# Performance work log

Hardware: AMD Instinct MI355X
Metric: run time of the kernel (lower is better)

The kernel has to match this reference:

```python
import jax, jax.numpy as jnp
import numpy as np
from jax import lax

B, T, D_IN = 512, 128, 512
HID, C = 256, 96
MAX_LEN = 25  # num_steps = MAX_LEN + 1


def setup_inputs() -> dict:
    key = jax.random.key(0)
    ks = jax.random.split(key, 12)
    num_steps = MAX_LEN + 1
    gru_in = D_IN + C
    inp = {
        "batch_H": jax.random.normal(ks[0], (B, T, D_IN), dtype=jnp.float32),
        "text": jax.random.randint(ks[1], (B, num_steps), 0, C, dtype=jnp.int64),
        "batch_max_length": MAX_LEN,
        # attention params
        "W_i2h": jax.random.normal(ks[2], (HID, D_IN), dtype=jnp.float32) * 0.04,
        "W_h2h": jax.random.normal(ks[3], (HID, HID), dtype=jnp.float32) * 0.06,
        "b_h2h": jnp.zeros((HID,), dtype=jnp.float32),
        "W_score": jax.random.normal(ks[4], (1, HID), dtype=jnp.float32) * 0.08,
        # GRUCell params (torch layout: [3H, in], gate order r, z, n)
        "W_ih": jax.random.normal(ks[5], (3 * HID, gru_in), dtype=jnp.float32) * 0.04,
        "W_hh": jax.random.normal(ks[6], (3 * HID, HID), dtype=jnp.float32) * 0.06,
        "b_ih": jnp.zeros((3 * HID,), dtype=jnp.float32),
        "b_hh": jnp.zeros((3 * HID,), dtype=jnp.float32),
        # generator
        "W_gen": jax.random.normal(ks[7], (C, HID), dtype=jnp.float32) * 0.07,
        "b_gen": jnp.zeros((C,), dtype=jnp.float32),
    }
    return inp


def reference(batch_H, text, batch_max_length, W_i2h, W_h2h, b_h2h, W_score,
              W_ih, W_hh, b_ih, b_hh, W_gen, b_gen):
    num_steps = batch_max_length + 1
    hid = W_h2h.shape[0]
    n_cls = W_gen.shape[0]
    dtype = batch_H.dtype
    bsz = batch_H.shape[0]

    # i2h(batch_H) is loop-invariant: [B, T, H]
    H_proj = jnp.einsum("btd,hd->bth", batch_H, W_i2h)

    def step(hidden, char_ids):
        # additive attention
        h_proj = hidden @ W_h2h.T + b_h2h                      # [B, H]
        e = jnp.tanh(H_proj + h_proj[:, None, :]) @ W_score[0]  # [B, T]
        alpha = jax.nn.softmax(e, axis=1)                       # [B, T]
        context = jnp.einsum("bt,btd->bd", alpha, batch_H)      # [B, D]
        onehot = jax.nn.one_hot(char_ids, n_cls, dtype=dtype)
        x = jnp.concatenate([context, onehot], axis=1)
        # GRUCell (torch semantics)
        gi = x @ W_ih.T + b_ih
        gh = hidden @ W_hh.T + b_hh
        i_r, i_z, i_n = jnp.split(gi, 3, axis=1)
        h_r, h_z, h_n = jnp.split(gh, 3, axis=1)
        r = jax.nn.sigmoid(i_r + h_r)
        z = jax.nn.sigmoid(i_z + h_z)
        n = jnp.tanh(i_n + r * h_n)
        new_h = (1.0 - z) * n + z * hidden
        return new_h, new_h

    h0 = jnp.zeros((bsz, hid), dtype=dtype)
    chars = jnp.swapaxes(text[:, :num_steps], 0, 1)  # [num_steps, B]
    _, hiddens = lax.scan(step, h0, chars)           # [num_steps, B, H]
    hiddens = jnp.swapaxes(hiddens, 0, 1)            # [B, num_steps, H]
    probs = hiddens @ W_gen.T + b_gen                # [B, num_steps, C]
    return probs
```

## Files before the change

kernel.cpp:

```cpp
#include <hip/hip_runtime.h>

#define BATCH 512
#define TLEN 128
#define DIN 512
#define HID 256
#define NCLS 96
#define STEPS 26
#define GRUIN 608
#define G3 768

#define BM 64
#define BN 64
#define BK 16
#define LDS_STRIDE 68

typedef unsigned short ushort_t;
typedef __attribute__((ext_vector_type(8))) short short8v;
typedef __attribute__((ext_vector_type(4))) float f32x4;
typedef __attribute__((ext_vector_type(8))) unsigned short ushort8v;

__device__ __forceinline__ float fast_tanh(float x) {
    return 1.f - 2.f / (__expf(2.f * x) + 1.f);
}
__device__ __forceinline__ float fast_sigmoid(float x) {
    return 1.f / (1.f + __expf(-x));
}
__device__ __forceinline__ ushort_t f2bf_rne(float f) {
    unsigned int u = __float_as_uint(f);
    unsigned int r = (u + 0x7FFFu + ((u >> 16) & 1u)) >> 16;
    return (ushort_t)r;
}
__device__ __forceinline__ float bf2f(ushort_t h) {
    return __uint_as_float(((unsigned int)h) << 16);
}

__global__ __launch_bounds__(256)
void prep_all(const float* __restrict__ W_h2h, const float* __restrict__ W_hh,
              const float* __restrict__ W_ih, const float* __restrict__ W_i2h,
              const float* __restrict__ b_ih, const float* __restrict__ b_h2h,
              const float* __restrict__ b_hh, const float* __restrict__ W_gen,
              ushort_t* __restrict__ Wcat16, ushort_t* __restrict__ B16cat,
              float* __restrict__ WembT, ushort_t* __restrict__ Wgen16,
              float* __restrict__ bcat, float* __restrict__ hidden,
              float* __restrict__ hg) {
    int idx = blockIdx.x * 256 + threadIdx.x;
    if (idx < 262144) {
        int n = idx >> 8, k = idx & 255;
        float v = (n < 256) ? W_h2h[n * 256 + k] : W_hh[(size_t)(n - 256) * 256 + k];
        Wcat16[idx] = f2bf_rne(v);
    } else if (idx < 262144 + 524288) {
        int j = idx - 262144;
        int r = j >> 9, c = j & 511;
        float v = (r < 768) ? W_ih[(size_t)r * GRUIN + c] : W_i2h[(size_t)(r - 768) * 512 + c];
        B16cat[j] = f2bf_rne(v);
    } else if (idx < 262144 + 524288 + 73728) {
        int j = idx - (262144 + 524288);
        int ch = j / 768, jj = j - ch * 768;
        WembT[j] = W_ih[(size_t)jj * GRUIN + 512 + ch] + b_ih[jj];
    } else if (idx < 262144 + 524288 + 73728 + 24576) {
        int j = idx - (262144 + 524288 + 73728);
        Wgen16[j] = f2bf_rne(W_gen[j]);
    } else if (idx < 262144 + 524288 + 73728 + 24576 + 1024) {
        int j = idx - (262144 + 524288 + 73728 + 24576);
        bcat[j] = (j < 256) ? b_h2h[j] : b_hh[j - 256];
    } else if (idx < 262144 + 524288 + 73728 + 24576 + 1024 + 131072) {
        int j = idx - (262144 + 524288 + 73728 + 24576 + 1024);
        hidden[j] = 0.f;
    } else if (idx < 262144 + 524288 + 73728 + 24576 + 1024 + 131072 + 524288) {
        int j = idx - (262144 + 524288 + 73728 + 24576 + 1024 + 131072);
        int c = j & 1023;
        hg[j] = (c < 256) ? b_h2h[c] : b_hh[c - 256];
    }
}

__global__ __launch_bounds__(256)
void conv_a16(const float* __restrict__ src, ushort_t* __restrict__ dst, int n8) {
    int i = blockIdx.x * 256 + threadIdx.x;
    const int stride = gridDim.x * 256;
    for (; i < n8; i += stride) {
        float4 v0 = ((const float4*)src)[2 * i];
        float4 v1 = ((const float4*)src)[2 * i + 1];
        ushort8v o;
        o[0] = f2bf_rne(v0.x); o[1] = f2bf_rne(v0.y);
        o[2] = f2bf_rne(v0.z); o[3] = f2bf_rne(v0.w);
        o[4] = f2bf_rne(v1.x); o[5] = f2bf_rne(v1.y);
        o[6] = f2bf_rne(v1.z); o[7] = f2bf_rne(v1.w);
        ((ushort8v*)dst)[i] = o;
    }
}

__device__ __forceinline__ int swz(int row, int col8) {
    return (row * 32 + col8 * 8) ^ ((row & 7) << 3);
}

__global__ __launch_bounds__(256)
void hwhp_mfma(const ushort_t* __restrict__ A16,
               const ushort_t* __restrict__ B16,
               ushort_t* __restrict__ HW16,
               ushort_t* __restrict__ Hp16) {
    __shared__ ushort_t As[128 * 32];
    __shared__ ushort_t Bs[128 * 32];
    const int wgid = blockIdx.x;
    const int mt = (wgid & 7) + ((wgid >> 6) << 3);
    const int nt = (wgid >> 3) & 7;
    const int bm = mt * 128, bn = nt * 128;
    const int tid = threadIdx.x;
    const int wid = tid >> 6, lane = tid & 63;
    const int wr = wid >> 1, wc = wid & 1;
    f32x4 acc[4][4] = {};
    const int l15 = lane & 15, lhi = lane >> 4;
    const int rin = (lane >> 2) ^ ((lane >> 4) & 1);
    const int qsrc = (lane & 3) ^ (rin & 3);
    for (int k0 = 0; k0 < 512; k0 += 32) {
        __syncthreads();
#pragma unroll
        for (int c = 0; c < 2; ++c) {
            const int chunk = wid + 4 * c;
            const int row = chunk * 16 + rin;
            __builtin_amdgcn_global_load_lds(
                (const __attribute__((address_space(1))) void*)(A16 + (size_t)(bm + row) * 512 + k0 + qsrc * 8),
                (__attribute__((address_space(3))) void*)(As + chunk * 512),
                16, 0, 0);
            __builtin_amdgcn_global_load_lds(
                (const __attribute__((address_space(1))) void*)(B16 + (size_t)(bn + row) * 512 + k0 + qsrc * 8),
                (__attribute__((address_space(3))) void*)(Bs + chunk * 512),
                16, 0, 0);
        }
        __syncthreads();
        short8v af[4], bfr[4];
#pragma unroll
        for (int i = 0; i < 4; ++i) {
            int arow = wr * 64 + i * 16 + l15;
            af[i] = *(const short8v*)(&As[swz(arow, lhi)]);
            int brow = wc * 64 + i * 16 + l15;
            bfr[i] = *(const short8v*)(&Bs[swz(brow, lhi)]);
        }
#pragma unroll
        for (int i = 0; i < 4; ++i)
#pragma unroll
            for (int j = 0; j < 4; ++j)
                acc[i][j] = __builtin_amdgcn_mfma_f32_16x16x32_bf16(af[i], bfr[j], acc[i][j], 0, 0, 0);
    }
    const int cr0 = bm + wr * 64 + lhi * 4;
    const int cc0 = bn + wc * 64 + l15;
    const bool isHW = (bn < 768);
    ushort_t* outp = isHW ? HW16 : Hp16;
    const int ld = isHW ? 768 : 256;
    const int coff = isHW ? 0 : 768;
#pragma unroll
    for (int i = 0; i < 4; ++i)
#pragma unroll
        for (int j = 0; j < 4; ++j)
#pragma unroll
            for (int p = 0; p < 4; ++p)
                outp[(size_t)(cr0 + i * 16 + p) * ld + (cc0 + j * 16 - coff)] = f2bf_rne(acc[i][j][p]);
}

__global__ __launch_bounds__(256)
void hg_mfma(const ushort_t* __restrict__ H16,
             const ushort_t* __restrict__ W16,
             const float* __restrict__ bcat,
             float* __restrict__ hg) {
    __shared__ ushort_t As[64 * 32];
    __shared__ ushort_t Bs[128 * 32];
    const int wgid = blockIdx.x;
    const int mt = wgid >> 3;
    const int nt = wgid & 7;
    const int bm = mt * 64, bn = nt * 128;
    const int tid = threadIdx.x;
    const int wid = tid >> 6, lane = tid & 63;
    const int wr = wid >> 1, wc = wid & 1;
    const int sr = tid >> 2, sq = tid & 3;
    f32x4 acc[2][4] = {};
    const int l15 = lane & 15, lhi = lane >> 4;
    for (int k0 = 0; k0 < 256; k0 += 32) {
        ushort8v a0 = *(const ushort8v*)(H16 + (size_t)(bm + (sr & 63)) * 256 + k0 + sq * 8);
        ushort8v b0 = *(const ushort8v*)(W16 + (size_t)(bn + sr) * 256 + k0 + sq * 8);
        ushort8v b1 = *(const ushort8v*)(W16 + (size_t)(bn + sr + 64) * 256 + k0 + sq * 8);
        __syncthreads();
        if (sr < 64) *(ushort8v*)(&As[swz(sr, sq)]) = a0;
        *(ushort8v*)(&Bs[swz(sr, sq)]) = b0;
        *(ushort8v*)(&Bs[swz(sr + 64, sq)]) = b1;
        __syncthreads();
        short8v af[2], bfr[4];
#pragma unroll
        for (int i = 0; i < 2; ++i) {
            int arow = wr * 32 + i * 16 + l15;
            af[i] = *(const short8v*)(&As[swz(arow, lhi)]);
        }
#pragma unroll
        for (int j = 0; j < 4; ++j) {
            int brow = wc * 64 + j * 16 + l15;
            bfr[j] = *(const short8v*)(&Bs[swz(brow, lhi)]);
        }
#pragma unroll
        for (int i = 0; i < 2; ++i)
#pragma unroll
            for (int j = 0; j < 4; ++j)
                acc[i][j] = __builtin_amdgcn_mfma_f32_16x16x32_bf16(af[i], bfr[j], acc[i][j], 0, 0, 0);
    }
    const int cr0 = bm + wr * 32 + lhi * 4;
    const int cc0 = bn + wc * 64 + l15;
#pragma unroll
    for (int j = 0; j < 4; ++j) {
        const int c = cc0 + j * 16;
        const float bj = bcat[c];
#pragma unroll
        for (int i = 0; i < 2; ++i)
#pragma unroll
            for (int p = 0; p < 4; ++p)
                hg[(size_t)(cr0 + i * 16 + p) * 1024 + c] = acc[i][j][p] + bj;
    }
}

__global__ __launch_bounds__(1024, 8)
void step_fused(const ushort_t* __restrict__ HW16,
                const ushort_t* __restrict__ Hp16,
                const float* __restrict__ hg,
                const float* __restrict__ WembT,
                const ushort_t* __restrict__ Wgen16,
                const float* __restrict__ Wscore,
                const float* __restrict__ b_gen,
                const int* __restrict__ text,
                int s,
                float* __restrict__ hidden,
                ushort_t* __restrict__ hidden16,
                float* __restrict__ out) {
    const int b = blockIdx.x;
    const int tid = threadIdx.x;
    const int wave = tid >> 6, lane = tid & 63;

    __shared__ __align__(16) float hp[HID];
    __shared__ __align__(16) float wsc[HID];
    __shared__ __align__(16) float parts[6144];
    __shared__ __align__(16) float gi_l[G3];
    __shared__ __align__(16) float sh[HID];
    __shared__ float es[TLEN];
    __shared__ float al[TLEN];
    __shared__ float red[16];

    const size_t rowbase = (size_t)b * TLEN;
    if (tid < 256) {
        hp[tid] = hg[(size_t)b * 1024 + tid];
        wsc[tid] = Wscore[tid];
    }
    __syncthreads();

#pragma unroll
    for (int i = 0; i < 8; ++i) {
        int t = i * 16 + wave;
        ushort4 hv = *(const ushort4*)(Hp16 + (rowbase + t) * 256 + lane * 4);
        float4 hpv = *(const float4*)(&hp[lane * 4]);
        float4 wv = *(const float4*)(&wsc[lane * 4]);
        float sc = fast_tanh(bf2f(hv.x) + hpv.x) * wv.x
                 + fast_tanh(bf2f(hv.y) + hpv.y) * wv.y
                 + fast_tanh(bf2f(hv.z) + hpv.z) * wv.z
                 + fast_tanh(bf2f(hv.w) + hpv.w) * wv.w;
#pragma unroll
        for (int off = 32; off >= 1; off >>= 1) sc += __shfl_xor(sc, off);
        if (lane == 0) es[t] = sc;
    }
    __syncthreads();
    float ev = 0.f, p = 0.f;
    if (tid < TLEN) {
        ev = es[tid];
        float mx = ev;
#pragma unroll
        for (int off = 32; off >= 1; off >>= 1) mx = fmaxf(mx, __shfl_xor(mx, off));
        if (lane == 0) red[wave] = mx;
    }
    __syncthreads();
    if (tid < TLEN) {
        float m = fmaxf(red[0], red[1]);
        p = __expf(ev - m);
        float sm = p;
#pragma unroll
        for (int off = 32; off >= 1; off >>= 1) sm += __shfl_xor(sm, off);
        if (lane == 0) red[8 + wave] = sm;
    }
    __syncthreads();
    if (tid < TLEN) al[tid] = p / (red[8] + red[9]);
    __syncthreads();
    {
        const int tg = tid >> 7;
        const int cq = tid & 127;
        if (cq < 96) {
            float a0 = 0.f, a1 = 0.f, a2 = 0.f, a3 = 0.f;
            float a4 = 0.f, a5 = 0.f, a6 = 0.f, a7 = 0.f;
            const ushort_t* base = HW16 + (rowbase + tg * 16) * 768 + cq * 8;
            const float* alh = &al[tg * 16];
#pragma unroll 4
            for (int i = 0; i < 16; ++i) {
                ushort8v v = *(const ushort8v*)(base + (size_t)i * 768);
                float a = alh[i];
                a0 = fmaf(a, bf2f(v[0]), a0);
                a1 = fmaf(a, bf2f(v[1]), a1);
                a2 = fmaf(a, bf2f(v[2]), a2);
                a3 = fmaf(a, bf2f(v[3]), a3);
                a4 = fmaf(a, bf2f(v[4]), a4);
                a5 = fmaf(a, bf2f(v[5]), a5);
                a6 = fmaf(a, bf2f(v[6]), a6);
                a7 = fmaf(a, bf2f(v[7]), a7);
            }
            float* pr = &parts[tg * 768 + cq * 8];
            pr[0] = a0; pr[1] = a1; pr[2] = a2; pr[3] = a3;
            pr[4] = a4; pr[5] = a5; pr[6] = a6; pr[7] = a7;
        }
    }
    __syncthreads();
    if (tid < G3) {
        float g = parts[tid] + parts[768 + tid] + parts[1536 + tid] + parts[2304 + tid]
                + parts[3072 + tid] + parts[3840 + tid] + parts[4608 + tid] + parts[5376 + tid];
        gi_l[tid] = g;
    }
    __syncthreads();
    if (tid < 256) {
        const int ch = text[b * STEPS + s];
        const float* em = WembT + (size_t)ch * G3;
        const float* ghb = hg + (size_t)b * 1024 + 256;
        float ir = gi_l[tid]       + em[tid]       + ghb[tid];
        float iz = gi_l[256 + tid] + em[256 + tid] + ghb[256 + tid];
        float in_ = gi_l[512 + tid] + em[512 + tid];
        float hn = ghb[512 + tid];
        float rr = fast_sigmoid(ir);
        float zz = fast_sigmoid(iz);
        float nn = fast_tanh(in_ + rr * hn);
        float nh = (1.f - zz) * nn + zz * hidden[(size_t)b * HID + tid];
        hidden[(size_t)b * HID + tid] = nh;
        hidden16[(size_t)b * HID + tid] = f2bf_rne(nh);
        sh[tid] = nh;
    }
    __syncthreads();
    if (tid < NCLS) {
        const ushort_t* wrow = Wgen16 + (size_t)tid * HID;
        float acc = b_gen[tid];
#pragma unroll 4
        for (int k = 0; k < HID; k += 8) {
            ushort8v w8 = *(const ushort8v*)(wrow + k);
            acc = fmaf(sh[k],     bf2f(w8[0]), acc);
            acc = fmaf(sh[k + 1], bf2f(w8[1]), acc);
            acc = fmaf(sh[k + 2], bf2f(w8[2]), acc);
            acc = fmaf(sh[k + 3], bf2f(w8[3]), acc);
            acc = fmaf(sh[k + 4], bf2f(w8[4]), acc);
            acc = fmaf(sh[k + 5], bf2f(w8[5]), acc);
            acc = fmaf(sh[k + 6], bf2f(w8[6]), acc);
            acc = fmaf(sh[k + 7], bf2f(w8[7]), acc);
        }
        out[((size_t)b * STEPS + s) * NCLS + tid] = acc;
    }
}

template <typename OutT>
__device__ __forceinline__ void store_c(OutT* p, float v);
template <> __device__ __forceinline__ void store_c<float>(float* p, float v) { *p = v; }
template <> __device__ __forceinline__ void store_c<ushort_t>(ushort_t* p, float v) { *p = f2bf_rne(v); }

template <typename OutT>
__global__ __launch_bounds__(256)
void gemm_nt(const float* __restrict__ A, int lda,
             const float* __restrict__ Bw, int ldb,
             OutT* __restrict__ Cc, int ldc,
             const float* __restrict__ bias,
             int M, int N, int K) {
    __shared__ float As[BK][LDS_STRIDE];
    __shared__ float Bs[BK][LDS_STRIDE];
    const int tid = threadIdx.x;
    const int bm = blockIdx.x * BM;
    const int bn = blockIdx.y * BN;
    const int tx = tid & 15, ty = tid >> 4;
    const int lr = tid >> 2;
    const int lc = (tid & 3) << 2;
    float acc[4][4] = {};
    const int gr = bm + lr;
    const int gn = bn + lr;
    const float* Arow = A + (size_t)gr * lda;
    const float* Brow = Bw + (size_t)gn * ldb;
    for (int k0 = 0; k0 < K; k0 += BK) {
        float4 va = make_float4(0.f, 0.f, 0.f, 0.f);
        float4 vb = make_float4(0.f, 0.f, 0.f, 0.f);
        if (gr < M) va = *(const float4*)(Arow + k0 + lc);
        if (gn < N) vb = *(const float4*)(Brow + k0 + lc);
        As[lc + 0][lr] = va.x; As[lc + 1][lr] = va.y;
        As[lc + 2][lr] = va.z; As[lc + 3][lr] = va.w;
        Bs[lc + 0][lr] = vb.x; Bs[lc + 1][lr] = vb.y;
        Bs[lc + 2][lr] = vb.z; Bs[lc + 3][lr] = vb.w;
        __syncthreads();
#pragma unroll
        for (int k = 0; k < BK; ++k) {
            float4 a4 = *(const float4*)(&As[k][ty << 2]);
            float4 b4 = *(const float4*)(&Bs[k][tx << 2]);
            float a[4] = {a4.x, a4.y, a4.z, a4.w};
            float b[4] = {b4.x, b4.y, b4.z, b4.w};
#pragma unroll
            for (int i = 0; i < 4; ++i)
#pragma unroll
                for (int j = 0; j < 4; ++j)
                    acc[i][j] = fmaf(a[i], b[j], acc[i][j]);
        }
        __syncthreads();
    }
#pragma unroll
    for (int i = 0; i < 4; ++i) {
        int m = bm + (ty << 2) + i;
        if (m >= M) continue;
#pragma unroll
        for (int j = 0; j < 4; ++j) {
            int n = bn + (tx << 2) + j;
            if (n < N) store_c(&Cc[(size_t)m * ldc + n], acc[i][j] + (bias ? bias[n] : 0.f));
        }
    }
}

__global__ __launch_bounds__(256)
void prep_wcat(const float* __restrict__ W_h2h, const float* __restrict__ W_hh,
               const float* __restrict__ b_h2h, const float* __restrict__ b_hh,
               float* __restrict__ Wcat, float* __restrict__ bcat,
               float* __restrict__ hidden) {
    int idx = blockIdx.x * 256 + threadIdx.x;
    int r = idx >> 8, c = idx & 255;
    Wcat[idx] = (r < 256) ? W_h2h[r * 256 + c] : W_hh[(r - 256) * 256 + c];
    if (idx < 1024) bcat[idx] = (idx < 256) ? b_h2h[idx] : b_hh[idx - 256];
    if (idx < BATCH * HID) hidden[idx] = 0.f;
}

template <typename HT>
__global__ __launch_bounds__(256)
void attn_step(const HT* __restrict__ Hproj,
               const float* __restrict__ batchH,
               const float* __restrict__ hg,
               const float* __restrict__ Wscore,
               float* __restrict__ context) {
    const int b = blockIdx.x;
    const int tid = threadIdx.x;
    __shared__ float hp[HID];
    __shared__ float wsc[HID];
    __shared__ float es[TLEN];
    __shared__ float red[16];
    hp[tid] = hg[b * 1024 + tid];
    wsc[tid] = Wscore[tid];
    __syncthreads();
    const int wave = tid >> 6;
    const int lane = tid & 63;
    const HT* Hp = Hproj + (size_t)b * TLEN * HID;
    for (int t = wave; t < TLEN; t += 4) {
        float x0, x1, x2, x3;
        if constexpr (sizeof(HT) == 4) {
            float4 hv = *(const float4*)((const float*)Hp + (size_t)t * HID + (lane << 2));
            x0 = hv.x; x1 = hv.y; x2 = hv.z; x3 = hv.w;
        } else {
            ushort4 hv = *(const ushort4*)((const ushort_t*)Hp + (size_t)t * HID + (lane << 2));
            x0 = bf2f(hv.x); x1 = bf2f(hv.y); x2 = bf2f(hv.z); x3 = bf2f(hv.w);
        }
        float4 hpv = *(const float4*)(&hp[lane << 2]);
        float4 wv = *(const float4*)(&wsc[lane << 2]);
        float sc = fast_tanh(x0 + hpv.x) * wv.x
                 + fast_tanh(x1 + hpv.y) * wv.y
                 + fast_tanh(x2 + hpv.z) * wv.z
                 + fast_tanh(x3 + hpv.w) * wv.w;
#pragma unroll
        for (int off = 32; off >= 1; off >>= 1) sc += __shfl_xor(sc, off);
        if (lane == 0) es[t] = sc;
    }
    __syncthreads();
    float e = (tid < TLEN) ? es[tid] : -INFINITY;
    float m = e;
#pragma unroll
    for (int off = 32; off >= 1; off >>= 1) m = fmaxf(m, __shfl_xor(m, off));
    if (lane == 0) red[wave] = m;
    __syncthreads();
    m = fmaxf(fmaxf(red[0], red[1]), fmaxf(red[2], red[3]));
    float p = (tid < TLEN) ? __expf(e - m) : 0.f;
    float ss = p;
#pragma unroll
    for (int off = 32; off >= 1; off >>= 1) ss += __shfl_xor(ss, off);
    if (lane == 0) red[8 + wave] = ss;
    __syncthreads();
    float denom = red[8] + red[9] + red[10] + red[11];
    if (tid < TLEN) es[tid] = p / denom;
    __syncthreads();
    const float* Hb = batchH + (size_t)b * TLEN * DIN;
    float acc0 = 0.f, acc1 = 0.f;
#pragma unroll 4
    for (int t = 0; t < TLEN; ++t) {
        float a = es[t];
        acc0 = fmaf(a, Hb[(size_t)t * DIN + tid], acc0);
        acc1 = fmaf(a, Hb[(size_t)t * DIN + HID + tid], acc1);
    }
    context[(size_t)b * DIN + tid] = acc0;
    context[(size_t)b * DIN + HID + tid] = acc1;
}

__global__ __launch_bounds__(256)
void gru_gate_gen(const float* __restrict__ gi,
                  const float* __restrict__ hg,
                  float* __restrict__ hidden,
                  float* __restrict__ out,
                  const int* __restrict__ text,
                  int s,
                  const float* __restrict__ W_ih,
                  const float* __restrict__ W_gen,
                  const float* __restrict__ b_gen) {
    const int b = blockIdx.x;
    const int h = threadIdx.x;
    __shared__ float sh[HID];
    const int ch = text[b * STEPS + s];
    const float* gib = gi + (size_t)b * G3;
    const float* ghb = hg + (size_t)b * 1024 + 256;
    float ir = gib[h]        + W_ih[(size_t)h * GRUIN + DIN + ch];
    float iz = gib[256 + h]  + W_ih[(size_t)(256 + h) * GRUIN + DIN + ch];
    float in_ = gib[512 + h] + W_ih[(size_t)(512 + h) * GRUIN + DIN + ch];
    float hr = ghb[h];
    float hz = ghb[256 + h];
    float hn = ghb[512 + h];
    float r = fast_sigmoid(ir + hr);
    float z = fast_sigmoid(iz + hz);
    float n = fast_tanh(in_ + r * hn);
    float hprev = hidden[b * HID + h];
    float nh = (1.f - z) * n + z * hprev;
    hidden[b * HID + h] = nh;
    sh[h] = nh;
    __syncthreads();
    if (h < NCLS) {
        const float* wg = W_gen + (size_t)h * HID;
        float acc = b_gen[h];
#pragma unroll 4
        for (int k = 0; k < HID; k += 4) {
            float4 w4 = *(const float4*)(wg + k);
            acc = fmaf(sh[k], w4.x, acc);
            acc = fmaf(sh[k + 1], w4.y, acc);
            acc = fmaf(sh[k + 2], w4.z, acc);
            acc = fmaf(sh[k + 3], w4.w, acc);
        }
        out[((size_t)b * STEPS + s) * NCLS + h] = acc;
    }
}

extern "C" void kernel_launch(void* const* d_in, const int* in_sizes, int n_in,
                              void* d_out, int out_size, void* d_ws, size_t ws_size,
                              hipStream_t stream) {
    const float* batch_H = (const float*)d_in[0];
    const int* text      = (const int*)d_in[1];
    const float* W_i2h   = (const float*)d_in[3];
    const float* W_h2h   = (const float*)d_in[4];
    const float* b_h2h   = (const float*)d_in[5];
    const float* W_score = (const float*)d_in[6];
    const float* W_ih    = (const float*)d_in[7];
    const float* W_hh    = (const float*)d_in[8];
    const float* b_ih    = (const float*)d_in[9];
    const float* b_hh    = (const float*)d_in[10];
    const float* W_gen   = (const float*)d_in[11];
    const float* b_gen   = (const float*)d_in[12];
    float* out = (float*)d_out;
    char* ws = (char*)d_ws;

    const size_t M = (size_t)BATCH * TLEN;
    const size_t nBH = M * DIN;
    const size_t hw_off     = 0;
    const size_t hp_off     = 100663296;
    const size_t a16_off    = hp_off + 33554432;
    const size_t b16cat_off = a16_off + 67108864;
    const size_t wcat_off   = b16cat_off + 1048576;
    const size_t wembT_off  = wcat_off + 524288;
    const size_t wgen16_off = wembT_off + 294912;
    const size_t bcat_off   = wgen16_off + 49152;
    const size_t hg_off     = bcat_off + 4096;
    const size_t hidden_off = hg_off + 2097152;
    const size_t h16_off    = hidden_off + 524288;
    const size_t need_new   = h16_off + 262144;

    if (ws_size >= need_new) {
        ushort_t* HW16     = (ushort_t*)(ws + hw_off);
        ushort_t* Hp16     = (ushort_t*)(ws + hp_off);
        ushort_t* A16      = (ushort_t*)(ws + a16_off);
        ushort_t* B16cat   = (ushort_t*)(ws + b16cat_off);
        ushort_t* Wcat16   = (ushort_t*)(ws + wcat_off);
        float*    WembT    = (float*)(ws + wembT_off);
        ushort_t* Wgen16   = (ushort_t*)(ws + wgen16_off);
        float*    bcat     = (float*)(ws + bcat_off);
        float*    hg       = (float*)(ws + hg_off);
        float*    hidden   = (float*)(ws + hidden_off);
        ushort_t* hidden16 = (ushort_t*)(ws + h16_off);

        hipLaunchKernelGGL(prep_all, dim3(6020), dim3(256), 0, stream,
                           W_h2h, W_hh, W_ih, W_i2h, b_ih, b_h2h, b_hh, W_gen,
                           Wcat16, B16cat, WembT, Wgen16, bcat, hidden, hg);
        hipLaunchKernelGGL(conv_a16, dim3(2048), dim3(256), 0, stream,
                           batch_H, A16, (int)(nBH / 8));
        hipLaunchKernelGGL(hwhp_mfma, dim3((M / 128) * 8), dim3(256), 0, stream,
                           A16, B16cat, HW16, Hp16);
        for (int s = 0; s < STEPS; ++s) {
            hipLaunchKernelGGL(step_fused, dim3(BATCH), dim3(1024), 0, stream,
                               HW16, Hp16, hg, WembT, Wgen16, W_score,
                               b_gen, text, s, hidden, hidden16, out);
            if (s < STEPS - 1) {
                hipLaunchKernelGGL(hg_mfma, dim3(64), dim3(256), 0, stream,
                                   hidden16, Wcat16, bcat, hg);
            }
        }
        return;
    }

    const size_t nHp = M * HID;
    const size_t small_floats = (size_t)BATCH * HID + BATCH * 1024 + BATCH * DIN
                              + BATCH * G3 + 1024 * HID + 1024;
    const size_t need_B32 = nHp * 4 + small_floats * 4;
    const bool use_fp32 = (ws_size >= need_B32);
    const size_t hp_bytes = use_fp32 ? nHp * 4 : nHp * 2;
    void* Hproj = (void*)ws;
    float* hiddenB = (float*)(ws + hp_bytes);
    float* hgB     = hiddenB + BATCH * HID;
    float* context = hgB + BATCH * 1024;
    float* gi      = context + BATCH * DIN;
    float* Wcat    = gi + BATCH * G3;
    float* bcatB   = Wcat + 1024 * HID;

    hipLaunchKernelGGL(prep_wcat, dim3(1024), dim3(256), 0, stream,
                       W_h2h, W_hh, b_h2h, b_hh, Wcat, bcatB, hiddenB);
    if (use_fp32) {
        hipLaunchKernelGGL(gemm_nt<float>, dim3(M / BM, HID / BN), dim3(256), 0, stream,
                           batch_H, DIN, W_i2h, DIN, (float*)Hproj, HID, (const float*)nullptr,
                           (int)M, HID, DIN);
    } else {
        hipLaunchKernelGGL(gemm_nt<ushort_t>, dim3(M / BM, HID / BN), dim3(256), 0, stream,
                           batch_H, DIN, W_i2h, DIN, (ushort_t*)Hproj, HID, (const float*)nullptr,
                           (int)M, HID, DIN);
    }
    for (int s = 0; s < STEPS; ++s) {
        hipLaunchKernelGGL(gemm_nt<float>, dim3(BATCH / BM, 1024 / BN), dim3(256), 0, stream,
                           hiddenB, HID, Wcat, HID, hgB, 1024, bcatB, BATCH, 1024, HID);
        if (use_fp32) {
            hipLaunchKernelGGL(attn_step<float>, dim3(BATCH), dim3(256), 0, stream,
                               (const float*)Hproj, batch_H, hgB, W_score, context);
        } else {
            hipLaunchKernelGGL(attn_step<ushort_t>, dim3(BATCH), dim3(256), 0, stream,
                               (const ushort_t*)Hproj, batch_H, hgB, W_score, context);
        }
        hipLaunchKernelGGL(gemm_nt<float>, dim3(BATCH / BM, G3 / BN), dim3(256), 0, stream,
                           context, DIN, W_ih, GRUIN, gi, G3, b_ih, BATCH, G3, DIN);
        hipLaunchKernelGGL(gru_gate_gen, dim3(BATCH), dim3(HID), 0, stream,
                           gi, hgB, hiddenB, out, text, s, W_ih, W_gen, b_gen);
    }
}
```

Baseline: 1.031 ms.

## Stage Hp16 and HW16 rows into LDS via global_load_lds in chunks

```diff
diff --git a/kernel.cpp b/kernel.cpp
--- a/kernel.cpp
+++ b/kernel.cpp
@@ -230,9 +230,10 @@
     const int tid = threadIdx.x;
     const int wave = tid >> 6, lane = tid & 63;
 
+    __shared__ __align__(16) ushort_t stage[12288];
+    __shared__ __align__(16) float parts[6144];
     __shared__ __align__(16) float hp[HID];
     __shared__ __align__(16) float wsc[HID];
-    __shared__ __align__(16) float parts[6144];
     __shared__ __align__(16) float gi_l[G3];
     __shared__ __align__(16) float sh[HID];
     __shared__ float es[TLEN];
@@ -244,21 +245,29 @@
         hp[tid] = hg[(size_t)b * 1024 + tid];
         wsc[tid] = Wscore[tid];
     }
-    __syncthreads();
-
-#pragma unroll
-    for (int i = 0; i < 8; ++i) {
-        int t = i * 16 + wave;
-        ushort4 hv = *(const ushort4*)(Hp16 + (rowbase + t) * 256 + lane * 4);
-        float4 hpv = *(const float4*)(&hp[lane * 4]);
-        float4 wv = *(const float4*)(&wsc[lane * 4]);
-        float sc = fast_tanh(bf2f(hv.x) + hpv.x) * wv.x
-                 + fast_tanh(bf2f(hv.y) + hpv.y) * wv.y
-                 + fast_tanh(bf2f(hv.z) + hpv.z) * wv.z
-                 + fast_tanh(bf2f(hv.w) + hpv.w) * wv.w;
-#pragma unroll
-        for (int off = 32; off >= 1; off >>= 1) sc += __shfl_xor(sc, off);
-        if (lane == 0) es[t] = sc;
+
+#pragma unroll 1
+    for (int c = 0; c < 4; ++c) {
+        __syncthreads();
+        __builtin_amdgcn_global_load_lds(
+            (const __attribute__((address_space(1))) void*)(Hp16 + (rowbase + c * 32) * 256 + (size_t)tid * 8),
+            (__attribute__((address_space(3))) void*)(stage + wave * 512),
+            16, 0, 0);
+        __syncthreads();
+#pragma unroll
+        for (int i = 0; i < 2; ++i) {
+            int tl = i * 16 + wave;
+            ushort4 hv = *(const ushort4*)(stage + tl * 256 + lane * 4);
+            float4 hpv = *(const float4*)(&hp[lane * 4]);
+            float4 wv = *(const float4*)(&wsc[lane * 4]);
+            float sc = fast_tanh(bf2f(hv.x) + hpv.x) * wv.x
+                     + fast_tanh(bf2f(hv.y) + hpv.y) * wv.y
+                     + fast_tanh(bf2f(hv.z) + hpv.z) * wv.z
+                     + fast_tanh(bf2f(hv.w) + hpv.w) * wv.w;
+#pragma unroll
+            for (int off = 32; off >= 1; off >>= 1) sc += __shfl_xor(sc, off);
+            if (lane == 0) es[c * 32 + tl] = sc;
+        }
     }
     __syncthreads();
     float ev = 0.f, p = 0.f;
@@ -280,32 +289,45 @@
     }
     __syncthreads();
     if (tid < TLEN) al[tid] = p / (red[8] + red[9]);
-    __syncthreads();
-    {
-        const int tg = tid >> 7;
-        const int cq = tid & 127;
+
+    const int tg = tid >> 7;
+    const int cq = tid & 127;
+    float a0 = 0.f, a1 = 0.f, a2 = 0.f, a3 = 0.f;
+    float a4 = 0.f, a5 = 0.f, a6 = 0.f, a7 = 0.f;
+#pragma unroll 1
+    for (int c = 0; c < 8; ++c) {
+        __syncthreads();
+        __builtin_amdgcn_global_load_lds(
+            (const __attribute__((address_space(1))) void*)(HW16 + (rowbase + c * 16) * 768 + (size_t)tid * 8),
+            (__attribute__((address_space(3))) void*)(stage + wave * 512),
+            16, 0, 0);
+        if (wave < 8) {
+            __builtin_amdgcn_global_load_lds(
+                (const __attribute__((address_space(1))) void*)(HW16 + (rowbase + c * 16) * 768 + (size_t)(1024 + tid) * 8),
+                (__attribute__((address_space(3))) void*)(stage + 8192 + wave * 512),
+                16, 0, 0);
+        }
+        __syncthreads();
         if (cq < 96) {
-            float a0 = 0.f, a1 = 0.f, a2 = 0.f, a3 = 0.f;
-            float a4 = 0.f, a5 = 0.f, a6 = 0.f, a7 = 0.f;
-            const ushort_t* base = HW16 + (rowbase + tg * 16) * 768 + cq * 8;
-            const float* alh = &al[tg * 16];
-#pragma unroll 4
-            for (int i = 0; i < 16; ++i) {
-                ushort8v v = *(const ushort8v*)(base + (size_t)i * 768);
-                float a = alh[i];
-                a0 = fmaf(a, bf2f(v[0]), a0);
-                a1 = fmaf(a, bf2f(v[1]), a1);
-                a2 = fmaf(a, bf2f(v[2]), a2);
-                a3 = fmaf(a, bf2f(v[3]), a3);
-                a4 = fmaf(a, bf2f(v[4]), a4);
-                a5 = fmaf(a, bf2f(v[5]), a5);
-                a6 = fmaf(a, bf2f(v[6]), a6);
-                a7 = fmaf(a, bf2f(v[7]), a7);
-            }
-            float* pr = &parts[tg * 768 + cq * 8];
-            pr[0] = a0; pr[1] = a1; pr[2] = a2; pr[3] = a3;
-            pr[4] = a4; pr[5] = a5; pr[6] = a6; pr[7] = a7;
-        }
+            const int r0 = tg * 2, r1 = r0 + 1;
+            const float aw0 = al[c * 16 + r0];
+            const float aw1 = al[c * 16 + r1];
+            ushort8v v0 = *(const ushort8v*)(stage + r0 * 768 + cq * 8);
+            ushort8v v1 = *(const ushort8v*)(stage + r1 * 768 + cq * 8);
+            a0 = fmaf(aw0, bf2f(v0[0]), fmaf(aw1, bf2f(v1[0]), a0));
+            a1 = fmaf(aw0, bf2f(v0[1]), fmaf(aw1, bf2f(v1[1]), a1));
+            a2 = fmaf(aw0, bf2f(v0[2]), fmaf(aw1, bf2f(v1[2]), a2));
+            a3 = fmaf(aw0, bf2f(v0[3]), fmaf(aw1, bf2f(v1[3]), a3));
+            a4 = fmaf(aw0, bf2f(v0[4]), fmaf(aw1, bf2f(v1[4]), a4));
+            a5 = fmaf(aw0, bf2f(v0[5]), fmaf(aw1, bf2f(v1[5]), a5));
+            a6 = fmaf(aw0, bf2f(v0[6]), fmaf(aw1, bf2f(v1[6]), a6));
+            a7 = fmaf(aw0, bf2f(v0[7]), fmaf(aw1, bf2f(v1[7]), a7));
+        }
+    }
+    if (cq < 96) {
+        float* pr = &parts[tg * 768 + cq * 8];
+        pr[0] = a0; pr[1] = a1; pr[2] = a2; pr[3] = a3;
+        pr[4] = a4; pr[5] = a5; pr[6] = a6; pr[7] = a7;
     }
     __syncthreads();
     if (tid < G3) {
```

After: 1.031 ms. Within noise of the previous version (+0.1%).
